# Kernel optimization log

Hardware: AMD Instinct MI355X
Metric: run time of the kernel (lower is better)

## Reference

```python
import jax, jax.numpy as jnp
import numpy as np

PRE, POST, BATCH, HIST = 1024, 1024, 256, 50
CONN_PROB = 0.1

def setup_inputs() -> dict:
    key = jax.random.key(0)
    k1, k2, k3, k4, k5 = jax.random.split(key, 5)
    pre_spikes = (jax.random.uniform(k1, (BATCH, PRE)) < 0.2).astype(jnp.float32)   # sparse spike trains
    post_spikes = (jax.random.uniform(k2, (BATCH, POST)) < 0.2).astype(jnp.float32)
    connectivity_mask = (jax.random.uniform(k3, (PRE, POST)) < CONN_PROB).astype(jnp.float32)
    synaptic_weights = jax.random.normal(k4, (PRE, POST), dtype=jnp.float32) * 0.1 * connectivity_mask
    correlation_history = jax.random.normal(k5, (PRE, POST, HIST), dtype=jnp.float32) * 0.01
    return {
        "pre_spikes": pre_spikes,
        "post_spikes": post_spikes,
        "synaptic_weights": synaptic_weights,
        "connectivity_mask": connectivity_mask,
        "correlation_history": correlation_history,
        "pre_activity": jnp.zeros((PRE,), jnp.float32),
        "post_activity": jnp.zeros((POST,), jnp.float32),
        "corr_index": 7,
    }

def reference(pre_spikes, post_spikes, synaptic_weights, connectivity_mask,
              correlation_history, pre_activity, post_activity, corr_index):
    # EMA of population activity (buffer updates in the torch module)
    pre_mean = pre_spikes.mean(axis=0)    # [pre]
    post_mean = post_spikes.mean(axis=0)  # [post]
    new_pre_activity = 0.99 * pre_activity + 0.01 * pre_mean
    new_post_activity = 0.99 * post_activity + 0.01 * post_mean

    # circular-buffer scatter: write current outer-product correlation at slot idx
    idx = corr_index % correlation_history.shape[-1]
    current_correlation = jnp.outer(pre_mean, post_mean)            # [pre, post]
    new_history = correlation_history.at[:, :, idx].set(current_correlation)

    # masked matmul: fuse elementwise mask into the GEMM operand
    effective_weights = synaptic_weights * connectivity_mask        # [pre, post]
    synaptic_current = pre_spikes @ effective_weights               # [batch, post]

    # connectivity_info['average_correlation'] (plasticity disabled: current_time <= 1.0)
    average_correlation = new_history.mean(axis=-1)                 # [pre, post]

    return (synaptic_current, new_pre_activity, new_post_activity,
            average_correlation, new_history)
```

## Files before the change

### kernel.cpp

```cpp
#include <hip/hip_runtime.h>

#define PRE   1024
#define POST  1024
#define BATCH 256
#define HIST  50
#define NPAIR (PRE * POST)

typedef float nf4 __attribute__((ext_vector_type(4)));

__global__ __launch_bounds__(256) void means_kernel(
    const float* __restrict__ pre_spikes,
    const float* __restrict__ post_spikes,
    const float* __restrict__ pre_activity,
    const float* __restrict__ post_activity,
    float* __restrict__ ws_means,
    float* __restrict__ out_pre_act,
    float* __restrict__ out_post_act)
{
    __shared__ float red[256];
    int tid = threadIdx.x;
    int blk = blockIdx.x;
    bool is_pre = blk < 16;
    const float* mat = is_pre ? pre_spikes : post_spikes;
    const float* act = is_pre ? pre_activity : post_activity;
    float* out_act   = is_pre ? out_pre_act : out_post_act;
    float* ws        = is_pre ? ws_means : ws_means + PRE;
    int col0 = (blk & 15) * 64;

    int col = col0 + (tid & 63);
    int chunk = tid >> 6;
    float s = 0.f;
#pragma unroll 8
    for (int r = chunk * 64; r < chunk * 64 + 64; ++r)
        s += mat[r * 1024 + col];
    red[tid] = s;
    __syncthreads();
    if (tid < 64) {
        float t = red[tid] + red[tid + 64] + red[tid + 128] + red[tid + 192];
        float m = t * (1.0f / BATCH);
        ws[col] = m;
        out_act[col] = 0.99f * act[col] + 0.01f * m;
    }
}

#define GBM 64
#define GBN 64
#define GBK 16
#define GKSPLIT 8
#define GLD 68
__global__ __launch_bounds__(256) void gemm_kernel(
    const float* __restrict__ A,
    const float* __restrict__ W,
    const float* __restrict__ Mk,
    float* __restrict__ C)
{
    __shared__ __align__(16) float As[GBK * GLD];
    __shared__ __align__(16) float Bs[GBK * GLD];
    int tid = threadIdx.x;
    int bn = blockIdx.x;
    int bm = blockIdx.y;
    int bz = blockIdx.z;
    int kbase = bz * (PRE / GKSPLIT);

    int ar = tid >> 2;
    int ak = (tid & 3) << 2;
    int bk = tid >> 4;
    int bn4 = (tid & 15) << 2;
    int tn4 = (tid & 15) << 2;
    int tm4 = (tid >> 4) << 2;

    const float* Ap = &A[(bm * GBM + ar) * PRE + kbase + ak];
    const float* Wp = &W [(size_t)(kbase + bk) * POST + bn * GBN + bn4];
    const float* Mp = &Mk[(size_t)(kbase + bk) * POST + bn * GBN + bn4];

    float acc[4][4] = {};

    for (int k0 = 0; k0 < PRE / GKSPLIT; k0 += GBK) {
        float4 av = *(const float4*)(Ap + k0);
        float4 wv = *(const float4*)(Wp + (size_t)k0 * POST);
        float4 mv = *(const float4*)(Mp + (size_t)k0 * POST);
        wv.x *= mv.x; wv.y *= mv.y; wv.z *= mv.z; wv.w *= mv.w;
        __syncthreads();
        As[(ak + 0) * GLD + ar] = av.x;
        As[(ak + 1) * GLD + ar] = av.y;
        As[(ak + 2) * GLD + ar] = av.z;
        As[(ak + 3) * GLD + ar] = av.w;
        *(float4*)&Bs[bk * GLD + bn4] = wv;
        __syncthreads();
#pragma unroll
        for (int kk = 0; kk < GBK; ++kk) {
            float4 a4 = *(const float4*)&As[kk * GLD + tm4];
            float4 b4 = *(const float4*)&Bs[kk * GLD + tn4];
            const float* ap = (const float*)&a4;
            const float* bp = (const float*)&b4;
#pragma unroll
            for (int i = 0; i < 4; ++i)
#pragma unroll
                for (int j = 0; j < 4; ++j)
                    acc[i][j] += ap[i] * bp[j];
        }
    }
#pragma unroll
    for (int i = 0; i < 4; ++i)
#pragma unroll
        for (int j = 0; j < 4; ++j)
            atomicAdd(&C[(size_t)(bm * GBM + tm4 + i) * POST + bn * GBN + tn4 + j],
                      acc[i][j]);
}

#define PPB 128
#define HTHREADS 320
#define NIT 5
__global__ __launch_bounds__(HTHREADS) void history_kernel(
    const float* __restrict__ hist_in,
    const int*   __restrict__ corr_index,
    const float* __restrict__ ws_means,
    float* __restrict__ hist_out,
    float* __restrict__ avg_out)
{
    __shared__ __align__(16) float tile[PPB * HIST];
    int tid = threadIdx.x;
    int p0 = blockIdx.x * PPB;
    int idx = ((corr_index[0] % HIST) + HIST) % HIST;

    const nf4* in4   = (const nf4*)(hist_in + (size_t)p0 * HIST);
    nf4*       out4  = (nf4*)(hist_out + (size_t)p0 * HIST);
    nf4*       tile4 = (nf4*)tile;

    nf4 v[NIT];
#pragma unroll
    for (int it = 0; it < NIT; ++it)
        v[it] = __builtin_nontemporal_load(&in4[it * HTHREADS + tid]);

#pragma unroll
    for (int it = 0; it < NIT; ++it) {
        int fl = it * HTHREADS + tid;
        int r0 = 4 * fl;
        int pl = r0 / HIST;
        int t0 = r0 - pl * HIST;
        int d  = idx - t0;
        int d2 = idx + HIST - t0;
        int pairA = p0 + pl;
        int pairB = pairA + 1;
        float corrA = ws_means[pairA >> 10] * ws_means[PRE + (pairA & (POST - 1))];
        float corrB = ws_means[(pairB >> 10) & 1023] * ws_means[PRE + (pairB & (POST - 1))];
        nf4 w = v[it];
        w.x = (d == 0) ? corrA : w.x;
        w.y = (d == 1) ? corrA : ((d2 == 1) ? corrB : w.y);
        w.z = (d == 2) ? corrA : ((d2 == 2) ? corrB : w.z);
        w.w = (d == 3) ? corrA : ((d2 == 3) ? corrB : w.w);
        tile4[fl] = w;
        __builtin_nontemporal_store(w, &out4[fl]);
    }
    __syncthreads();

    if (tid < PPB) {
        int pair = p0 + tid;
        const float2* tp = (const float2*)&tile[tid * HIST];
        float s = 0.f;
#pragma unroll
        for (int k = 0; k < HIST / 2; ++k) {
            float2 w = tp[k];
            s += w.x + w.y;
        }
        __builtin_nontemporal_store(s * (1.0f / HIST), &avg_out[pair]);
    }
}

extern "C" void kernel_launch(void* const* d_in, const int* in_sizes, int n_in,
                              void* d_out, int out_size, void* d_ws, size_t ws_size,
                              hipStream_t stream)
{
    const float* pre_spikes  = (const float*)d_in[0];
    const float* post_spikes = (const float*)d_in[1];
    const float* W           = (const float*)d_in[2];
    const float* Mk          = (const float*)d_in[3];
    const float* hist        = (const float*)d_in[4];
    const float* pre_act     = (const float*)d_in[5];
    const float* post_act    = (const float*)d_in[6];
    const int*   corr_index  = (const int*)d_in[7];

    float* out = (float*)d_out;
    float* out_current  = out;
    float* out_pre_act  = out + 262144;
    float* out_post_act = out + 263168;
    float* out_avg      = out + 264192;
    float* out_hist     = out + 1312768;

    float* ws_means = (float*)d_ws;

    means_kernel<<<32, 256, 0, stream>>>(
        pre_spikes, post_spikes, pre_act, post_act,
        ws_means, out_pre_act, out_post_act);

    (void)hipMemsetAsync(out_current, 0, (size_t)BATCH * POST * sizeof(float), stream);

    gemm_kernel<<<dim3(POST / GBN, BATCH / GBM, GKSPLIT), 256, 0, stream>>>(
        pre_spikes, W, Mk, out_current);

    history_kernel<<<NPAIR / PPB, HTHREADS, 0, stream>>>(
        hist, corr_index, ws_means, out_hist, out_avg);
}
```

Measured before the change: 410.5 us.

## Replace history smem tile with shared atomic partial sums; widen means grid

The history kernel drops its 25.6KB shared tile that was used to reduce each pair's 50-element window. Threads now accumulate partial sums per float4 straight into a 128-float shared array using shared-memory atomics, and only load the correlation value when a slot actually needs it. The goal is higher occupancy and no second pass over LDS. Separately, the means kernel goes from 32 to 128 blocks with 16 columns each, which spreads the reduction across more CUs. The cost is contention on the LDS atomics, and the summation order changes, so floating-point results may differ slightly.

```diff
diff --git a/kernel.cpp b/kernel.cpp
--- a/kernel.cpp
+++ b/kernel.cpp
@@ -8,6 +8,7 @@
 
 typedef float nf4 __attribute__((ext_vector_type(4)));
 
+#define MCOLS 16
 __global__ __launch_bounds__(256) void means_kernel(
     const float* __restrict__ pre_spikes,
     const float* __restrict__ post_spikes,
@@ -20,26 +21,30 @@
     __shared__ float red[256];
     int tid = threadIdx.x;
     int blk = blockIdx.x;
-    bool is_pre = blk < 16;
+    bool is_pre = blk < 64;
     const float* mat = is_pre ? pre_spikes : post_spikes;
     const float* act = is_pre ? pre_activity : post_activity;
     float* out_act   = is_pre ? out_pre_act : out_post_act;
     float* ws        = is_pre ? ws_means : ws_means + PRE;
-    int col0 = (blk & 15) * 64;
-
-    int col = col0 + (tid & 63);
-    int chunk = tid >> 6;
+    int col0 = (blk & 63) * MCOLS;
+
+    int col = col0 + (tid & 15);
+    int chunk = tid >> 4;
     float s = 0.f;
-#pragma unroll 8
-    for (int r = chunk * 64; r < chunk * 64 + 64; ++r)
+#pragma unroll
+    for (int r = chunk * 16; r < chunk * 16 + 16; ++r)
         s += mat[r * 1024 + col];
     red[tid] = s;
     __syncthreads();
-    if (tid < 64) {
-        float t = red[tid] + red[tid + 64] + red[tid + 128] + red[tid + 192];
+    if (tid < 16) {
+        float t = 0.f;
+#pragma unroll
+        for (int k = 0; k < 16; ++k)
+            t += red[k * 16 + tid];
         float m = t * (1.0f / BATCH);
-        ws[col] = m;
-        out_act[col] = 0.99f * act[col] + 0.01f * m;
+        int c = col0 + tid;
+        ws[c] = m;
+        out_act[c] = 0.99f * act[c] + 0.01f * m;
     }
 }
 
@@ -118,19 +123,22 @@
     float* __restrict__ hist_out,
     float* __restrict__ avg_out)
 {
-    __shared__ __align__(16) float tile[PPB * HIST];
+    __shared__ float psum[PPB];
     int tid = threadIdx.x;
     int p0 = blockIdx.x * PPB;
     int idx = ((corr_index[0] % HIST) + HIST) % HIST;
 
-    const nf4* in4   = (const nf4*)(hist_in + (size_t)p0 * HIST);
-    nf4*       out4  = (nf4*)(hist_out + (size_t)p0 * HIST);
-    nf4*       tile4 = (nf4*)tile;
+    if (tid < PPB) psum[tid] = 0.f;
+
+    const nf4* in4  = (const nf4*)(hist_in + (size_t)p0 * HIST);
+    nf4*       out4 = (nf4*)(hist_out + (size_t)p0 * HIST);
 
     nf4 v[NIT];
 #pragma unroll
     for (int it = 0; it < NIT; ++it)
         v[it] = __builtin_nontemporal_load(&in4[it * HTHREADS + tid]);
+
+    __syncthreads();
 
 #pragma unroll
     for (int it = 0; it < NIT; ++it) {
@@ -140,31 +148,34 @@
         int t0 = r0 - pl * HIST;
         int d  = idx - t0;
         int d2 = idx + HIST - t0;
-        int pairA = p0 + pl;
-        int pairB = pairA + 1;
-        float corrA = ws_means[pairA >> 10] * ws_means[PRE + (pairA & (POST - 1))];
-        float corrB = ws_means[(pairB >> 10) & 1023] * ws_means[PRE + (pairB & (POST - 1))];
+        bool strad = (t0 == 48);
+        bool needA = ((unsigned)d) < 4u;
+        bool needB = (d2 < 4);
+        float corr = 0.f;
+        if (needA | needB) {
+            int pair = needA ? (p0 + pl) : (p0 + pl + 1);
+            corr = ws_means[pair >> 10] * ws_means[PRE + (pair & (POST - 1))];
+        }
         nf4 w = v[it];
-        w.x = (d == 0) ? corrA : w.x;
-        w.y = (d == 1) ? corrA : ((d2 == 1) ? corrB : w.y);
-        w.z = (d == 2) ? corrA : ((d2 == 2) ? corrB : w.z);
-        w.w = (d == 3) ? corrA : ((d2 == 3) ? corrB : w.w);
-        tile4[fl] = w;
+        w.x = (d == 0) ? corr : w.x;
+        w.y = (d == 1) ? corr : w.y;
+        w.z = (d == 2 || d2 == 2) ? corr : w.z;
+        w.w = (d == 3 || d2 == 3) ? corr : w.w;
         __builtin_nontemporal_store(w, &out4[fl]);
+
+        float slo = w.x + w.y;
+        float shi = w.z + w.w;
+        if (strad) {
+            atomicAdd(&psum[pl], slo);
+            atomicAdd(&psum[pl + 1], shi);
+        } else {
+            atomicAdd(&psum[pl], slo + shi);
+        }
     }
     __syncthreads();
 
-    if (tid < PPB) {
-        int pair = p0 + tid;
-        const float2* tp = (const float2*)&tile[tid * HIST];
-        float s = 0.f;
-#pragma unroll
-        for (int k = 0; k < HIST / 2; ++k) {
-            float2 w = tp[k];
-            s += w.x + w.y;
-        }
-        __builtin_nontemporal_store(s * (1.0f / HIST), &avg_out[pair]);
-    }
+    if (tid < PPB)
+        __builtin_nontemporal_store(psum[tid] * (1.0f / HIST), &avg_out[p0 + tid]);
 }
 
 extern "C" void kernel_launch(void* const* d_in, const int* in_sizes, int n_in,
@@ -189,7 +200,7 @@
 
     float* ws_means = (float*)d_ws;
 
-    means_kernel<<<32, 256, 0, stream>>>(
+    means_kernel<<<128, 256, 0, stream>>>(
         pre_spikes, post_spikes, pre_act, post_act,
         ws_means, out_pre_act, out_post_act);
 
```

Result: slower. 436.0 us (+6.2%).
